# Performance work log

Measured on AMD Instinct MI355X. Metric: run time of the kernel, lower is better.

The kernel has to match this reference:

```python
import jax, jax.numpy as jnp
import numpy as np

H, DD, NCLS, NELEM, NPROP = 256, 32, 8, 11, 14
B, N = 4, 4096
ENC = NELEM + NPROP  # 25

_DIMS = [("dc1", ENC, H), ("dc21", H, DD), ("dc22", H, DD),
         ("in1", ENC, H), ("in2", H, H), ("in3", H, H),
         ("conv", H, H),
         ("id1", H, H), ("id2", H, H), ("id3", H, H),
         ("oid", H, NCLS), ("och", H, 2),
         ("m1", H + NCLS, H + NCLS), ("m2", H + NCLS, H), ("m3", H, H), ("om", H, 3)]


def setup_inputs() -> dict:
    key = jax.random.key(0)
    ks = jax.random.split(key, 2 + len(_DIMS))
    X = jax.random.normal(ks[0], (B, N, 15), jnp.float32)
    ids = jax.random.randint(ks[1], (B, N), 0, NELEM).astype(jnp.float32)
    X = X.at[:, :, 0].set(ids)
    d = {"X": X}
    for i, (name, di, do) in enumerate(_DIMS):
        W = jax.random.normal(ks[2 + i], (di, do), jnp.float32) / np.sqrt(di)
        d["W_" + name] = W
        d["b_" + name] = jnp.zeros((do,), jnp.float32)
    return d


def reference(X, W_dc1, b_dc1, W_dc21, b_dc21, W_dc22, b_dc22,
              W_in1, b_in1, W_in2, b_in2, W_in3, b_in3,
              W_conv, b_conv,
              W_id1, b_id1, W_id2, b_id2, W_id3, b_id3,
              W_oid, b_oid, W_och, b_och,
              W_m1, b_m1, W_m2, b_m2, W_m3, b_m3, W_om, b_om):
    act = jax.nn.selu
    # input encoding: one-hot element id (stop-grad via int cast) + properties, then selu
    onehot = jax.nn.one_hot(X[:, :, 0].astype(jnp.int32), NELEM, dtype=X.dtype)
    enc = act(jnp.concatenate([onehot, X[:, :, 1:]], axis=-1))  # [B,N,25]
    # distance coordinates
    h = act(enc @ W_dc1 + b_dc1)
    c1 = h @ W_dc21 + b_dc21  # [B,N,DD]
    c2 = h @ W_dc22 + b_dc22
    # pairwise distance -> exp adjacency
    na = jnp.sum(c1 * c1, -1)[:, :, None]
    nb = jnp.sum(c2 * c2, -1)[:, None, :]
    Dsq = jnp.clip(na - 2.0 * jnp.einsum('bnd,bmd->bnm', c1, c2) + nb, 1e-12, 1e12)
    adj = jnp.exp(-jnp.sqrt(Dsq))  # [B,N,N]
    # node MLP
    x = act(enc @ W_in1 + b_in1)
    x = act(x @ W_in2 + b_in2)
    x = act(x @ W_in3 + b_in3)
    # GraphConv: adj^k @ (x W) + b, k=4 (in-degree norm computed but unused upstream)
    x = act(jnp.einsum('bnm,bmh->bnh', adj ** 4, x @ W_conv) + b_conv)
    # id head
    a = act(x @ W_id1 + b_id1)
    a = act(a @ W_id2 + b_id2)
    a = act(a @ W_id3 + b_id3)
    out_id_logits = a @ W_oid + b_oid  # [B,N,8]
    out_charge = a @ W_och + b_och     # [B,N,2]
    # momentum head
    xb = jnp.concatenate([x, act(out_id_logits)], axis=-1)
    bb = act(xb @ W_m1 + b_m1)
    bb = act(bb @ W_m2 + b_m2)
    bb = act(bb @ W_m3 + b_m3)
    corr = bb @ W_om + b_om  # [B,N,3]
    mom = jnp.stack([X[:, :, 2] + corr[:, :, 0],
                     X[:, :, 3] + corr[:, :, 1],
                     X[:, :, 4] + corr[:, :, 2]], axis=-1)
    return jnp.concatenate([out_id_logits, mom, out_charge], axis=-1)  # [B,N,13]
```

## Files before the change

### kernel.cpp

```cpp
#include <hip/hip_runtime.h>
#include <cstddef>
#include <cstdint>

#define MROWS 16384
#define NSEQ  4096
#define ASTR  296
#define SELU_SCALE  1.0507009873554805f
#define SELU_ASCALE 1.7580993408473766f

typedef short bf16x8 __attribute__((ext_vector_type(8)));
typedef float f32x4  __attribute__((ext_vector_type(4)));

__device__ __forceinline__ float selu_f(float x) {
    return x > 0.f ? SELU_SCALE * x : SELU_ASCALE * (__expf(x) - 1.f);
}
__device__ __forceinline__ unsigned short f2bf(float x) {
    union { float f; unsigned int u; } v; v.f = x;
    unsigned int r = v.u + 0x7fffu + ((v.u >> 16) & 1u);
    return (unsigned short)(r >> 16);
}
__device__ __forceinline__ unsigned short t2bf(float x) {
    union { float f; unsigned int u; } v; v.f = x;
    return (unsigned short)(v.u >> 16);
}

struct PrepEnt { const float* W; unsigned short* WTf; int N, K, ntiles, KS, tileOff, tilesN; };
struct PrepArgs {
    PrepEnt e[16];
    const float *b21, *b22, *boid, *boch, *bdc1, *bin1;
    float *bc12, *boo, *bcat;
};
__global__ __launch_bounds__(256) void prep_kernel(PrepArgs pa) {
    if (blockIdx.y == 1) {
        if (blockIdx.x == 0) {
            int t = threadIdx.x;
            if (t < 32) pa.bc12[t] = pa.b21[t];
            else if (t < 64) pa.bc12[t] = pa.b22[t - 32];
            else if (t < 96) {
                int j = t - 64;
                pa.boo[j] = j < 8 ? pa.boid[j] : ((j >= 16 && j < 18) ? pa.boch[j - 16] : 0.f);
            }
        } else if (blockIdx.x == 1) {
            pa.bcat[threadIdx.x] = pa.bdc1[threadIdx.x];
        } else if (blockIdx.x == 2) {
            pa.bcat[256 + threadIdx.x] = pa.bin1[threadIdx.x];
        }
        return;
    }
    int bx = blockIdx.x;
    int ei = 0;
#pragma unroll
    for (int e = 1; e < 16; ++e)
        if (bx >= pa.e[e].tileOff) ei = e;
    PrepEnt E = pa.e[ei];
    int local = bx - E.tileOff;
    int tn = local / E.KS, tk = local - tn * E.KS;
    int k0 = tk * 32, n0 = tn * 32;

    __shared__ float ts[32][33];
    int t = threadIdx.x;
    {
        int kl = t >> 3, nl4 = (t & 7) * 4;
        int gk = k0 + kl;
#pragma unroll
        for (int j = 0; j < 4; ++j) {
            int gn = n0 + nl4 + j;
            float v = (gk < E.K && gn < E.N) ? E.W[(size_t)gk * E.N + gn] : 0.f;
            ts[nl4 + j][kl] = v;
        }
    }
    __syncthreads();
    int nl = t >> 3, kl4 = (t & 7) * 4;
    int n = n0 + nl;
    if (n < E.ntiles * 16) {
        ushort4 o;
        o.x = f2bf(ts[nl][kl4 + 0]);
        o.y = f2bf(ts[nl][kl4 + 1]);
        o.z = f2bf(ts[nl][kl4 + 2]);
        o.w = f2bf(ts[nl][kl4 + 3]);
        size_t dst = ((size_t)(n >> 4) * E.KS + tk) * 512 +
                     (size_t)((kl4 >> 3) * 16 + (n & 15)) * 8 + (kl4 & 7);
        *(ushort4*)(E.WTf + dst) = o;
    }
}

template <int MT, int NT>
__device__ __forceinline__ void zero_acc(f32x4 (&acc)[MT][NT]) {
#pragma unroll
    for (int i = 0; i < MT; ++i)
#pragma unroll
        for (int nt = 0; nt < NT; ++nt) acc[i][nt] = (f32x4){0.f, 0.f, 0.f, 0.f};
}

template <int MT, int NT, int K>
__device__ __forceinline__ void compute_tiles(
    f32x4 (&acc)[MT][NT],
    const unsigned short* __restrict__ src, int sstr,
    const unsigned short* __restrict__ WTf,
    int col0, int ln)
{
    constexpr int KS = (K + 31) / 32;
    int quad = ln >> 4, l15 = ln & 15;
    const unsigned short* wp = WTf + (size_t)(col0 >> 4) * (KS * 512) + ln * 8;
    bf16x8 st[3][NT];
#pragma unroll
    for (int s = 0; s < 3; ++s) {
        if (s < KS) {
#pragma unroll
            for (int nt = 0; nt < NT; ++nt)
                st[s][nt] = *(const bf16x8*)(wp + nt * (KS * 512) + s * 512);
        }
    }
#pragma unroll
    for (int ks = 0; ks < KS; ++ks) {
        bf16x8 bnew[NT];
        if (ks + 3 < KS) {
#pragma unroll
            for (int nt = 0; nt < NT; ++nt)
                bnew[nt] = *(const bf16x8*)(wp + nt * (KS * 512) + (ks + 3) * 512);
        }
#pragma unroll
        for (int i = 0; i < MT; ++i) {
            bf16x8 af = *(const bf16x8*)(src + (i * 16 + l15) * sstr + ks * 32 + quad * 8);
#pragma unroll
            for (int nt = 0; nt < NT; ++nt)
                acc[i][nt] = __builtin_amdgcn_mfma_f32_16x16x32_bf16(af, st[ks % 3][nt], acc[i][nt], 0, 0, 0);
        }
        if (ks + 3 < KS) {
#pragma unroll
            for (int nt = 0; nt < NT; ++nt) st[ks % 3][nt] = bnew[nt];
        }
    }
}

template <int MT, int NT>
__device__ __forceinline__ void store_tiles(
    f32x4 (&acc)[MT][NT], unsigned short* __restrict__ dst,
    int col0, const float* __restrict__ bias, int Nreal, int act, int ln)
{
    int quad = ln >> 4, l15 = ln & 15;
#pragma unroll
    for (int nt = 0; nt < NT; ++nt) {
        int col = col0 + nt * 16 + l15;
        float bv = (bias && col < Nreal) ? bias[col] : 0.f;
#pragma unroll
        for (int i = 0; i < MT; ++i) {
#pragma unroll
            for (int r = 0; r < 4; ++r) {
                int row = i * 16 + quad * 4 + r;
                float v = acc[i][nt][r] + bv;
                if (act) v = selu_f(v);
                if (col >= Nreal) v = 0.f;
                dst[row * ASTR + col] = f2bf(v);
            }
        }
    }
}

__global__ __launch_bounds__(512, 6) void pre_mega(
    const float* __restrict__ X,
    const unsigned short* __restrict__ WTdF, const float* __restrict__ bcat,
    const unsigned short* __restrict__ WTc12F, const float* __restrict__ bc12,
    const unsigned short* __restrict__ WTin2F, const float* __restrict__ b_in2,
    const unsigned short* __restrict__ WTin3F, const float* __restrict__ b_in3,
    const unsigned short* __restrict__ WTconvF,
    unsigned short* __restrict__ c1b, unsigned short* __restrict__ c2b,
    float* __restrict__ n1, float* __restrict__ n2,
    unsigned short* __restrict__ xwTb)
{
    __shared__ unsigned short encs[32 * 32];
    __shared__ unsigned short bufA[32 * ASTR];
    __shared__ unsigned short bufB[32 * ASTR];
    __shared__ float c12s[32 * 68];

    int tid = threadIdx.x, wv = tid >> 6, ln = tid & 63;
    int quad = ln >> 4, l15 = ln & 15;
    int row0 = blockIdx.x * 32;

#pragma unroll
    for (int p = 0; p < 2; ++p) {
        int idx = p * 512 + tid;
        int row = idx >> 5, col = idx & 31;
        float v = 0.f;
        if (col < 11) {
            int id = (int)X[(size_t)(row0 + row) * 15];
            v = (id == col) ? SELU_SCALE : 0.f;
        } else if (col < 25) {
            v = selu_f(X[(size_t)(row0 + row) * 15 + 1 + (col - 11)]);
        }
        encs[row * 32 + col] = f2bf(v);
    }
    __syncthreads();

#pragma unroll
    for (int ph = 0; ph < 2; ++ph) {
        f32x4 acc[2][2]; zero_acc<2, 2>(acc);
        compute_tiles<2, 2, 32>(acc, encs, 32, WTdF + (size_t)ph * 16 * 512, wv * 32, ln);
        store_tiles<2, 2>(acc, ph ? bufB : bufA, wv * 32, bcat + ph * 256, 256, 1, ln);
    }
    __syncthreads();

    f32x4 ax2[2][2]; zero_acc<2, 2>(ax2);
    compute_tiles<2, 2, 256>(ax2, bufB, ASTR, WTin2F, wv * 32, ln);
    f32x4 ac12[2][1];
    if (wv < 4) {
        zero_acc<2, 1>(ac12);
        compute_tiles<2, 1, 256>(ac12, bufA, ASTR, WTc12F, wv * 16, ln);
    }
    __syncthreads();
    store_tiles<2, 2>(ax2, bufA, wv * 32, b_in2, 256, 1, ln);
    if (wv < 4) {
        int col = wv * 16 + l15;
        float bv = bc12[col];
#pragma unroll
        for (int i = 0; i < 2; ++i)
#pragma unroll
            for (int r = 0; r < 4; ++r)
                c12s[(i * 16 + quad * 4 + r) * 68 + col] = ac12[i][0][r] + bv;
    }
    __syncthreads();

    if (tid < 32) {
        int grow = row0 + tid;
        const float* p = &c12s[tid * 68];
        float s1 = 0.f, s2 = 0.f;
        unsigned int o1[16], o2[16];
#pragma unroll
        for (int k = 0; k < 32; k += 2) {
            float a0 = p[k], a1 = p[k + 1];
            s1 += a0 * a0 + a1 * a1;
            o1[k >> 1] = (unsigned)f2bf(a0) | ((unsigned)f2bf(a1) << 16);
            float b0 = p[32 + k], b1 = p[33 + k];
            s2 += b0 * b0 + b1 * b1;
            o2[k >> 1] = (unsigned)f2bf(b0) | ((unsigned)f2bf(b1) << 16);
        }
        uint4* d1 = (uint4*)(c1b + (size_t)grow * 32);
        uint4* d2 = (uint4*)(c2b + (size_t)grow * 32);
#pragma unroll
        for (int j = 0; j < 4; ++j) {
            d1[j] = make_uint4(o1[4 * j], o1[4 * j + 1], o1[4 * j + 2], o1[4 * j + 3]);
            d2[j] = make_uint4(o2[4 * j], o2[4 * j + 1], o2[4 * j + 2], o2[4 * j + 3]);
        }
        n1[grow] = s1;
        n2[grow] = s2;
    }

    {
        f32x4 acc[2][2]; zero_acc<2, 2>(acc);
        compute_tiles<2, 2, 256>(acc, bufA, ASTR, WTin3F, wv * 32, ln);
        store_tiles<2, 2>(acc, bufB, wv * 32, b_in3, 256, 1, ln);
    }
    __syncthreads();
    {
        f32x4 acc[2][2]; zero_acc<2, 2>(acc);
        compute_tiles<2, 2, 256>(acc, bufB, ASTR, WTconvF, wv * 32, ln);
        store_tiles<2, 2>(acc, bufA, wv * 32, nullptr, 256, 0, ln);
    }
    __syncthreads();

    int b = row0 >> 12;
    int c0 = (row0 & 4095) >> 5;
    unsigned short* dst = xwTb + (size_t)(b * 128 + c0) * (256 * 32);
#pragma unroll
    for (int p = 0; p < 2; ++p) {
        int idx = p * 512 + tid;
        int h = idx >> 2, g = idx & 3;
        unsigned int w[4];
#pragma unroll
        for (int j = 0; j < 4; ++j) {
            unsigned int lo = bufA[(g * 8 + 2 * j) * ASTR + h];
            unsigned int hi = bufA[(g * 8 + 2 * j + 1) * ASTR + h];
            w[j] = lo | (hi << 16);
        }
        *(uint4*)(dst + (size_t)h * 32 + g * 8) = make_uint4(w[0], w[1], w[2], w[3]);
    }
}

__global__ __launch_bounds__(512, 4) void adj_conv_mfma(
    const unsigned short* __restrict__ c1b, const unsigned short* __restrict__ c2b,
    const float* __restrict__ n1, const float* __restrict__ n2,
    const unsigned short* __restrict__ xwTb, const float* __restrict__ bconv,
    unsigned short* __restrict__ xc)
{
    __shared__ unsigned short wls[2][32][136];

    int tid = threadIdx.x, wv = tid >> 6, ln = tid & 63, quad = ln >> 4, l15 = ln & 15;
    int blk = blockIdx.x;
    int b = (blk >> 1) & 3;
    int iidx = ((blk >> 3) << 1) | (blk & 1);
    int i0 = iidx * 32;
    size_t base = (size_t)b * NSEQ;

    bf16x8 c1f0 = *(const bf16x8*)(c1b + (base + i0 + l15) * 32 + quad * 8);
    bf16x8 c1f1 = *(const bf16x8*)(c1b + (base + i0 + 16 + l15) * 32 + quad * 8);
    float4 n1v0 = *(const float4*)(n1 + base + i0 + quad * 4);
    float4 n1v1 = *(const float4*)(n1 + base + i0 + 16 + quad * 4);

    const unsigned short* xwp0 = xwTb + (size_t)b * (128 * 256 * 32)
                               + ((size_t)(wv * 32 + l15) * 32 + quad * 8);
    const unsigned short* xwp1 = xwp0 + 8192;
    const unsigned short* xwp2 = xwp0 + 16384;
    const unsigned short* xwp3 = xwp0 + 24576;
    const unsigned short* c2p  = c2b + (base + wv * 16 + l15) * 32 + quad * 8;
    const float* n2p = n2 + base + wv * 16 + l15;

    f32x4 acc[2][2];
#pragma unroll
    for (int i = 0; i < 2; ++i)
#pragma unroll
        for (int j = 0; j < 2; ++j) acc[i][j] = (f32x4){0.f, 0.f, 0.f, 0.f};

    bf16x8 c2f = *(const bf16x8*)c2p;
    float nn2 = *n2p;
    c2p += 4096; n2p += 128;
    {
        f32x4 d0 = (f32x4){0.f, 0.f, 0.f, 0.f};
        f32x4 d1 = (f32x4){0.f, 0.f, 0.f, 0.f};
        d0 = __builtin_amdgcn_mfma_f32_16x16x32_bf16(c1f0, c2f, d0, 0, 0, 0);
        d1 = __builtin_amdgcn_mfma_f32_16x16x32_bf16(c1f1, c2f, d1, 0, 0, 0);
#pragma unroll
        for (int r = 0; r < 4; ++r) {
            float D0 = fmaf(-2.f, d0[r], n1v0[r] + nn2);
            float D1 = fmaf(-2.f, d1[r], n1v1[r] + nn2);
            float t0 = __builtin_amdgcn_sqrtf(fmaxf(D0, 1e-12f));
            float t1 = __builtin_amdgcn_sqrtf(fmaxf(D1, 1e-12f));
            wls[0][quad * 4 + r][wv * 16 + l15]      = t2bf(__expf(t0 * -4.f));
            wls[0][16 + quad * 4 + r][wv * 16 + l15] = t2bf(__expf(t1 * -4.f));
        }
    }
    c2f = *(const bf16x8*)c2p;
    nn2 = *n2p;
    c2p += 4096; n2p += 128;
    __syncthreads();

    for (int itr = 0; itr < 32; ++itr) {
        int p = itr & 1;
        bf16x8 bfc[4][2];
#pragma unroll
        for (int ht = 0; ht < 2; ++ht) {
            bfc[0][ht] = *(const bf16x8*)(xwp0 + ht * 512);
            bfc[1][ht] = *(const bf16x8*)(xwp1 + ht * 512);
            bfc[2][ht] = *(const bf16x8*)(xwp2 + ht * 512);
            bfc[3][ht] = *(const bf16x8*)(xwp3 + ht * 512);
        }
        xwp0 += 32768; xwp1 += 32768; xwp2 += 32768; xwp3 += 32768;

        if (itr < 31) {
            f32x4 d0 = (f32x4){0.f, 0.f, 0.f, 0.f};
            f32x4 d1 = (f32x4){0.f, 0.f, 0.f, 0.f};
            d0 = __builtin_amdgcn_mfma_f32_16x16x32_bf16(c1f0, c2f, d0, 0, 0, 0);
            d1 = __builtin_amdgcn_mfma_f32_16x16x32_bf16(c1f1, c2f, d1, 0, 0, 0);
            bf16x8 c2n; float nnn;
            if (itr < 30) {
                c2n = *(const bf16x8*)c2p;
                nnn = *n2p;
                c2p += 4096; n2p += 128;
            }
#pragma unroll
            for (int r = 0; r < 4; ++r) {
                float D0 = fmaf(-2.f, d0[r], n1v0[r] + nn2);
                float D1 = fmaf(-2.f, d1[r], n1v1[r] + nn2);
                float t0 = __builtin_amdgcn_sqrtf(fmaxf(D0, 1e-12f));
                float t1 = __builtin_amdgcn_sqrtf(fmaxf(D1, 1e-12f));
                wls[p ^ 1][quad * 4 + r][wv * 16 + l15]      = t2bf(__expf(t0 * -4.f));
                wls[p ^ 1][16 + quad * 4 + r][wv * 16 + l15] = t2bf(__expf(t1 * -4.f));
            }
            if (itr < 30) { c2f = c2n; nn2 = nnn; }
        }

#pragma unroll
        for (int ks = 0; ks < 4; ++ks) {
            bf16x8 af0 = *(const bf16x8*)&wls[p][l15][ks * 32 + quad * 8];
            bf16x8 af1 = *(const bf16x8*)&wls[p][16 + l15][ks * 32 + quad * 8];
            acc[0][0] = __builtin_amdgcn_mfma_f32_16x16x32_bf16(af0, bfc[ks][0], acc[0][0], 0, 0, 0);
            acc[0][1] = __builtin_amdgcn_mfma_f32_16x16x32_bf16(af0, bfc[ks][1], acc[0][1], 0, 0, 0);
            acc[1][0] = __builtin_amdgcn_mfma_f32_16x16x32_bf16(af1, bfc[ks][0], acc[1][0], 0, 0, 0);
            acc[1][1] = __builtin_amdgcn_mfma_f32_16x16x32_bf16(af1, bfc[ks][1], acc[1][1], 0, 0, 0);
        }
        __syncthreads();
    }

#pragma unroll
    for (int mi = 0; mi < 2; ++mi) {
#pragma unroll
        for (int ht = 0; ht < 2; ++ht) {
            int h = wv * 32 + ht * 16 + l15;
            float bv = bconv[h];
#pragma unroll
            for (int r = 0; r < 4; ++r) {
                int irow = i0 + mi * 16 + quad * 4 + r;
                xc[(base + irow) * 256 + h] = f2bf(selu_f(acc[mi][ht][r] + bv));
            }
        }
    }
}

__global__ __launch_bounds__(512, 4) void post_mega(
    const float* __restrict__ X, const unsigned short* __restrict__ xc,
    const unsigned short* __restrict__ WTid1F, const float* __restrict__ b_id1,
    const unsigned short* __restrict__ WTid2F, const float* __restrict__ b_id2,
    const unsigned short* __restrict__ WTid3F, const float* __restrict__ b_id3,
    const unsigned short* __restrict__ WTooF, const float* __restrict__ boo,
    const unsigned short* __restrict__ WTm1F, const float* __restrict__ b_m1,
    const unsigned short* __restrict__ WTm2F, const float* __restrict__ b_m2,
    const unsigned short* __restrict__ WTm3F, const float* __restrict__ b_m3,
    const unsigned short* __restrict__ WTomF, const float* __restrict__ b_om,
    float* __restrict__ out)
{
    __shared__ unsigned short xcs[32 * ASTR];
    __shared__ unsigned short bufA[32 * ASTR];
    __shared__ unsigned short bufB[32 * ASTR];
    __shared__ float lgs[32 * 32];

    int tid = threadIdx.x, wv = tid >> 6, ln = tid & 63;
    int quad = ln >> 4, l15 = ln & 15;
    int row0 = blockIdx.x * 32;

#pragma unroll
    for (int p = 0; p < 2; ++p) {
        int idx = p * 512 + tid;
        int row = idx >> 5, c8 = (idx & 31) * 8;
        *(uint4*)&xcs[row * ASTR + c8] = *(const uint4*)(xc + (size_t)(row0 + row) * 256 + c8);
    }
#pragma unroll
    for (int p = 0; p < 3; ++p) {
        int idx = p * 512 + tid;
        if (idx < 1280) {
            int row = idx / 40, c = 256 + idx - row * 40;
            xcs[row * ASTR + c] = 0;
            bufB[row * ASTR + c] = 0;
        }
    }
    __syncthreads();

    {
        f32x4 acc[2][2]; zero_acc<2, 2>(acc);
        compute_tiles<2, 2, 256>(acc, xcs, ASTR, WTid1F, wv * 32, ln);
        store_tiles<2, 2>(acc, bufA, wv * 32, b_id1, 256, 1, ln);
    }
    __syncthreads();
    {
        f32x4 acc[2][2]; zero_acc<2, 2>(acc);
        compute_tiles<2, 2, 256>(acc, bufA, ASTR, WTid2F, wv * 32, ln);
        store_tiles<2, 2>(acc, bufB, wv * 32, b_id2, 256, 1, ln);
    }
    __syncthreads();
    {
        f32x4 acc[2][2]; zero_acc<2, 2>(acc);
        compute_tiles<2, 2, 256>(acc, bufB, ASTR, WTid3F, wv * 32, ln);
        store_tiles<2, 2>(acc, bufA, wv * 32, b_id3, 256, 1, ln);
    }
    __syncthreads();
    if (wv == 0) {
        f32x4 acc[2][2]; zero_acc<2, 2>(acc);
        compute_tiles<2, 2, 256>(acc, bufA, ASTR, WTooF, 0, ln);
#pragma unroll
        for (int nt = 0; nt < 2; ++nt) {
            int col = nt * 16 + l15;
            float bv = boo[col];
#pragma unroll
            for (int i = 0; i < 2; ++i)
#pragma unroll
                for (int r = 0; r < 4; ++r)
                    lgs[(i * 16 + quad * 4 + r) * 32 + col] = acc[i][nt][r] + bv;
        }
    }
    __syncthreads();
    if (tid < 32) {
        float* op = out + (size_t)(row0 + tid) * 13;
#pragma unroll
        for (int c = 0; c < 8; ++c) {
            float lg = lgs[tid * 32 + c];
            op[c] = lg;
            xcs[tid * ASTR + 256 + c] = f2bf(selu_f(lg));
        }
        op[11] = lgs[tid * 32 + 16];
        op[12] = lgs[tid * 32 + 17];
    }
    __syncthreads();
    {
        f32x4 acc[2][2]; zero_acc<2, 2>(acc);
        compute_tiles<2, 2, 288>(acc, xcs, ASTR, WTm1F, wv * 32, ln);
        store_tiles<2, 2>(acc, bufB, wv * 32, b_m1, 264, 1, ln);
        if (wv == 1) {
            f32x4 acx[2][1]; zero_acc<2, 1>(acx);
            compute_tiles<2, 1, 288>(acx, xcs, ASTR, WTm1F, 256, ln);
            store_tiles<2, 1>(acx, bufB, 256, b_m1, 264, 1, ln);
        }
    }
    __syncthreads();
    {
        f32x4 acc[2][2]; zero_acc<2, 2>(acc);
        compute_tiles<2, 2, 288>(acc, bufB, ASTR, WTm2F, wv * 32, ln);
        store_tiles<2, 2>(acc, bufA, wv * 32, b_m2, 256, 1, ln);
    }
    __syncthreads();
    {
        f32x4 acc[2][2]; zero_acc<2, 2>(acc);
        compute_tiles<2, 2, 256>(acc, bufA, ASTR, WTm3F, wv * 32, ln);
        store_tiles<2, 2>(acc, bufB, wv * 32, b_m3, 256, 1, ln);
    }
    __syncthreads();
    if (wv == 0) {
        f32x4 acc[2][1]; zero_acc<2, 1>(acc);
        compute_tiles<2, 1, 256>(acc, bufB, ASTR, WTomF, 0, ln);
        if (l15 < 3) {
            float bv = b_om[l15];
#pragma unroll
            for (int i = 0; i < 2; ++i)
#pragma unroll
                for (int r = 0; r < 4; ++r) {
                    int grow = row0 + i * 16 + quad * 4 + r;
                    out[(size_t)grow * 13 + 8 + l15] =
                        X[(size_t)grow * 15 + 2 + l15] + acc[i][0][r] + bv;
                }
        }
    }
}

extern "C" void kernel_launch(void* const* d_in, const int* in_sizes, int n_in,
                              void* d_out, int out_size, void* d_ws, size_t ws_size,
                              hipStream_t stream) {
    (void)in_sizes; (void)n_in; (void)out_size; (void)ws_size;

    const float* X = (const float*)d_in[0];
    const float* W_dc1 = (const float*)d_in[1];  const float* b_dc1 = (const float*)d_in[2];
    const float* W_dc21 = (const float*)d_in[3]; const float* b_dc21 = (const float*)d_in[4];
    const float* W_dc22 = (const float*)d_in[5]; const float* b_dc22 = (const float*)d_in[6];
    const float* W_in1 = (const float*)d_in[7];  const float* b_in1 = (const float*)d_in[8];
    const float* W_in2 = (const float*)d_in[9];  const float* b_in2 = (const float*)d_in[10];
    const float* W_in3 = (const float*)d_in[11]; const float* b_in3 = (const float*)d_in[12];
    const float* W_conv = (const float*)d_in[13]; const float* b_conv = (const float*)d_in[14];
    const float* W_id1 = (const float*)d_in[15]; const float* b_id1 = (const float*)d_in[16];
    const float* W_id2 = (const float*)d_in[17]; const float* b_id2 = (const float*)d_in[18];
    const float* W_id3 = (const float*)d_in[19]; const float* b_id3 = (const float*)d_in[20];
    const float* W_oid = (const float*)d_in[21]; const float* b_oid = (const float*)d_in[22];
    const float* W_och = (const float*)d_in[23]; const float* b_och = (const float*)d_in[24];
    const float* W_m1 = (const float*)d_in[25];  const float* b_m1 = (const float*)d_in[26];
    const float* W_m2 = (const float*)d_in[27];  const float* b_m2 = (const float*)d_in[28];
    const float* W_m3 = (const float*)d_in[29];  const float* b_m3 = (const float*)d_in[30];
    const float* W_om = (const float*)d_in[31];  const float* b_om = (const float*)d_in[32];

    const size_t M = MROWS;
    char* pw = (char*)d_ws;
    auto alloc = [&](size_t bytes) -> void* {
        void* r = (void*)pw;
        pw += (bytes + 255) & ~(size_t)255;
        return r;
    };
    unsigned short* c1b = (unsigned short*)alloc(M * 32 * 2);
    unsigned short* c2b = (unsigned short*)alloc(M * 32 * 2);
    float* n1 = (float*)alloc(M * 4);
    float* n2 = (float*)alloc(M * 4);
    unsigned short* xwTb = (unsigned short*)alloc((size_t)4 * 128 * 256 * 32 * 2);
    unsigned short* xcb = (unsigned short*)alloc(M * 256 * 2);
    unsigned short* WTdF   = (unsigned short*)alloc((size_t)2 * 16 * 1 * 512 * 2);
    unsigned short* WTc12F = (unsigned short*)alloc((size_t)4 * 8 * 512 * 2);
    unsigned short* WTin2F = (unsigned short*)alloc((size_t)16 * 8 * 512 * 2);
    unsigned short* WTin3F = (unsigned short*)alloc((size_t)16 * 8 * 512 * 2);
    unsigned short* WTconvF = (unsigned short*)alloc((size_t)16 * 8 * 512 * 2);
    unsigned short* WTid1F = (unsigned short*)alloc((size_t)16 * 8 * 512 * 2);
    unsigned short* WTid2F = (unsigned short*)alloc((size_t)16 * 8 * 512 * 2);
    unsigned short* WTid3F = (unsigned short*)alloc((size_t)16 * 8 * 512 * 2);
    unsigned short* WTm3F  = (unsigned short*)alloc((size_t)16 * 8 * 512 * 2);
    unsigned short* WTooF  = (unsigned short*)alloc((size_t)2 * 8 * 512 * 2);
    unsigned short* WTm1F  = (unsigned short*)alloc((size_t)17 * 9 * 512 * 2);
    unsigned short* WTm2F  = (unsigned short*)alloc((size_t)16 * 9 * 512 * 2);
    unsigned short* WTomF  = (unsigned short*)alloc((size_t)1 * 8 * 512 * 2);
    float* bc12 = (float*)alloc(64 * 4);
    float* boo = (float*)alloc(32 * 4);
    float* bcat = (float*)alloc(512 * 4);

    PrepArgs pa;
    int off = 0;
    auto ent = [&](const float* W, unsigned short* WTf, int N, int K, int ntiles) {
        PrepEnt e; e.W = W; e.WTf = WTf; e.N = N; e.K = K; e.ntiles = ntiles;
        e.KS = (K + 31) / 32;
        e.tilesN = (ntiles * 16 + 31) / 32;
        e.tileOff = off;
        off += e.tilesN * e.KS;
        return e;
    };
    pa.e[0]  = ent(W_dc1,  WTdF,                256, 25,  16);
    pa.e[1]  = ent(W_in1,  WTdF + 16 * 512,     256, 25,  16);
    pa.e[2]  = ent(W_dc21, WTc12F,              32,  256, 2);
    pa.e[3]  = ent(W_dc22, WTc12F + 2 * 8 * 512, 32, 256, 2);
    pa.e[4]  = ent(W_in2,  WTin2F,              256, 256, 16);
    pa.e[5]  = ent(W_in3,  WTin3F,              256, 256, 16);
    pa.e[6]  = ent(W_conv, WTconvF,             256, 256, 16);
    pa.e[7]  = ent(W_id1,  WTid1F,              256, 256, 16);
    pa.e[8]  = ent(W_id2,  WTid2F,              256, 256, 16);
    pa.e[9]  = ent(W_id3,  WTid3F,              256, 256, 16);
    pa.e[10] = ent(W_m3,   WTm3F,               256, 256, 16);
    pa.e[11] = ent(W_oid,  WTooF,               8,   256, 1);
    pa.e[12] = ent(W_och,  WTooF + 8 * 512,     2,   256, 1);
    pa.e[13] = ent(W_m1,   WTm1F,               264, 264, 17);
    pa.e[14] = ent(W_m2,   WTm2F,               256, 264, 16);
    pa.e[15] = ent(W_om,   WTomF,               3,   256, 1);
    pa.b21 = b_dc21; pa.b22 = b_dc22; pa.boid = b_oid; pa.boch = b_och;
    pa.bdc1 = b_dc1; pa.bin1 = b_in1;
    pa.bc12 = bc12; pa.boo = boo; pa.bcat = bcat;
    prep_kernel<<<dim3(off, 2), 256, 0, stream>>>(pa);

    pre_mega<<<dim3(512), 512, 0, stream>>>(X, WTdF, bcat, WTc12F, bc12,
                                            WTin2F, b_in2, WTin3F, b_in3, WTconvF,
                                            c1b, c2b, n1, n2, xwTb);

    adj_conv_mfma<<<dim3(512), 512, 0, stream>>>(c1b, c2b, n1, n2, xwTb, b_conv, xcb);

    post_mega<<<dim3(512), 512, 0, stream>>>(X, xcb,
                                             WTid1F, b_id1, WTid2F, b_id2, WTid3F, b_id3,
                                             WTooF, boo, WTm1F, b_m1, WTm2F, b_m2,
                                             WTm3F, b_m3, WTomF, b_om, (float*)d_out);
}
```

Baseline: 241.5 us.

## Fuse adjacency-conv kernel with post-MLP heads into one kernel

Merges the adjacency/graph-conv kernel and the post MLP kernel so each block keeps its 32 conv output rows in shared memory and runs the id and momentum heads directly. This removes the global write and read of the 16384x256 bf16 intermediate and one kernel launch. In exchange, shared memory per block grows a lot (conv staging buffers plus three activation buffers), which can lower occupancy during the dominant N^2 adjacency phase.

```diff
diff --git a/kernel.cpp b/kernel.cpp
--- a/kernel.cpp
+++ b/kernel.cpp
@@ -276,13 +276,26 @@
     }
 }
 
-__global__ __launch_bounds__(512, 4) void adj_conv_mfma(
+__global__ __launch_bounds__(512, 4) void adj_post(
     const unsigned short* __restrict__ c1b, const unsigned short* __restrict__ c2b,
     const float* __restrict__ n1, const float* __restrict__ n2,
     const unsigned short* __restrict__ xwTb, const float* __restrict__ bconv,
-    unsigned short* __restrict__ xc)
+    const float* __restrict__ X,
+    const unsigned short* __restrict__ WTid1F, const float* __restrict__ b_id1,
+    const unsigned short* __restrict__ WTid2F, const float* __restrict__ b_id2,
+    const unsigned short* __restrict__ WTid3F, const float* __restrict__ b_id3,
+    const unsigned short* __restrict__ WTooF, const float* __restrict__ boo,
+    const unsigned short* __restrict__ WTm1F, const float* __restrict__ b_m1,
+    const unsigned short* __restrict__ WTm2F, const float* __restrict__ b_m2,
+    const unsigned short* __restrict__ WTm3F, const float* __restrict__ b_m3,
+    const unsigned short* __restrict__ WTomF, const float* __restrict__ b_om,
+    float* __restrict__ out)
 {
     __shared__ unsigned short wls[2][32][136];
+    __shared__ unsigned short xcs[32 * ASTR];
+    __shared__ unsigned short bufA[32 * ASTR];
+    __shared__ unsigned short bufB[32 * ASTR];
+    __shared__ float lgs[32 * 32];
 
     int tid = threadIdx.x, wv = tid >> 6, ln = tid & 63, quad = ln >> 4, l15 = ln & 15;
     int blk = blockIdx.x;
@@ -290,6 +303,17 @@
     int iidx = ((blk >> 3) << 1) | (blk & 1);
     int i0 = iidx * 32;
     size_t base = (size_t)b * NSEQ;
+    size_t grow0 = base + i0;
+
+#pragma unroll
+    for (int p = 0; p < 3; ++p) {
+        int idx = p * 512 + tid;
+        if (idx < 1280) {
+            int row = idx / 40, c = 256 + idx - row * 40;
+            xcs[row * ASTR + c] = 0;
+            bufB[row * ASTR + c] = 0;
+        }
+    }
 
     bf16x8 c1f0 = *(const bf16x8*)(c1b + (base + i0 + l15) * 32 + quad * 8);
     bf16x8 c1f1 = *(const bf16x8*)(c1b + (base + i0 + 16 + l15) * 32 + quad * 8);
@@ -388,72 +412,34 @@
             float bv = bconv[h];
 #pragma unroll
             for (int r = 0; r < 4; ++r) {
-                int irow = i0 + mi * 16 + quad * 4 + r;
-                xc[(base + irow) * 256 + h] = f2bf(selu_f(acc[mi][ht][r] + bv));
+                int lrow = mi * 16 + quad * 4 + r;
+                xcs[lrow * ASTR + h] = f2bf(selu_f(acc[mi][ht][r] + bv));
             }
         }
     }
-}
-
-__global__ __launch_bounds__(512, 4) void post_mega(
-    const float* __restrict__ X, const unsigned short* __restrict__ xc,
-    const unsigned short* __restrict__ WTid1F, const float* __restrict__ b_id1,
-    const unsigned short* __restrict__ WTid2F, const float* __restrict__ b_id2,
-    const unsigned short* __restrict__ WTid3F, const float* __restrict__ b_id3,
-    const unsigned short* __restrict__ WTooF, const float* __restrict__ boo,
-    const unsigned short* __restrict__ WTm1F, const float* __restrict__ b_m1,
-    const unsigned short* __restrict__ WTm2F, const float* __restrict__ b_m2,
-    const unsigned short* __restrict__ WTm3F, const float* __restrict__ b_m3,
-    const unsigned short* __restrict__ WTomF, const float* __restrict__ b_om,
-    float* __restrict__ out)
-{
-    __shared__ unsigned short xcs[32 * ASTR];
-    __shared__ unsigned short bufA[32 * ASTR];
-    __shared__ unsigned short bufB[32 * ASTR];
-    __shared__ float lgs[32 * 32];
-
-    int tid = threadIdx.x, wv = tid >> 6, ln = tid & 63;
-    int quad = ln >> 4, l15 = ln & 15;
-    int row0 = blockIdx.x * 32;
-
-#pragma unroll
-    for (int p = 0; p < 2; ++p) {
-        int idx = p * 512 + tid;
-        int row = idx >> 5, c8 = (idx & 31) * 8;
-        *(uint4*)&xcs[row * ASTR + c8] = *(const uint4*)(xc + (size_t)(row0 + row) * 256 + c8);
-    }
-#pragma unroll
-    for (int p = 0; p < 3; ++p) {
-        int idx = p * 512 + tid;
-        if (idx < 1280) {
-            int row = idx / 40, c = 256 + idx - row * 40;
-            xcs[row * ASTR + c] = 0;
-            bufB[row * ASTR + c] = 0;
-        }
-    }
-    __syncthreads();
-
-    {
-        f32x4 acc[2][2]; zero_acc<2, 2>(acc);
-        compute_tiles<2, 2, 256>(acc, xcs, ASTR, WTid1F, wv * 32, ln);
-        store_tiles<2, 2>(acc, bufA, wv * 32, b_id1, 256, 1, ln);
-    }
-    __syncthreads();
-    {
-        f32x4 acc[2][2]; zero_acc<2, 2>(acc);
-        compute_tiles<2, 2, 256>(acc, bufA, ASTR, WTid2F, wv * 32, ln);
-        store_tiles<2, 2>(acc, bufB, wv * 32, b_id2, 256, 1, ln);
-    }
-    __syncthreads();
-    {
-        f32x4 acc[2][2]; zero_acc<2, 2>(acc);
-        compute_tiles<2, 2, 256>(acc, bufB, ASTR, WTid3F, wv * 32, ln);
-        store_tiles<2, 2>(acc, bufA, wv * 32, b_id3, 256, 1, ln);
+    __syncthreads();
+
+    {
+        f32x4 a2[2][2]; zero_acc<2, 2>(a2);
+        compute_tiles<2, 2, 256>(a2, xcs, ASTR, WTid1F, wv * 32, ln);
+        store_tiles<2, 2>(a2, bufA, wv * 32, b_id1, 256, 1, ln);
+    }
+    __syncthreads();
+    {
+        f32x4 a2[2][2]; zero_acc<2, 2>(a2);
+        compute_tiles<2, 2, 256>(a2, bufA, ASTR, WTid2F, wv * 32, ln);
+        store_tiles<2, 2>(a2, bufB, wv * 32, b_id2, 256, 1, ln);
+    }
+    __syncthreads();
+    {
+        f32x4 a2[2][2]; zero_acc<2, 2>(a2);
+        compute_tiles<2, 2, 256>(a2, bufB, ASTR, WTid3F, wv * 32, ln);
+        store_tiles<2, 2>(a2, bufA, wv * 32, b_id3, 256, 1, ln);
     }
     __syncthreads();
     if (wv == 0) {
-        f32x4 acc[2][2]; zero_acc<2, 2>(acc);
-        compute_tiles<2, 2, 256>(acc, bufA, ASTR, WTooF, 0, ln);
+        f32x4 a2[2][2]; zero_acc<2, 2>(a2);
+        compute_tiles<2, 2, 256>(a2, bufA, ASTR, WTooF, 0, ln);
 #pragma unroll
         for (int nt = 0; nt < 2; ++nt) {
             int col = nt * 16 + l15;
@@ -462,12 +448,12 @@
             for (int i = 0; i < 2; ++i)
 #pragma unroll
                 for (int r = 0; r < 4; ++r)
-                    lgs[(i * 16 + quad * 4 + r) * 32 + col] = acc[i][nt][r] + bv;
+                    lgs[(i * 16 + quad * 4 + r) * 32 + col] = a2[i][nt][r] + bv;
         }
     }
     __syncthreads();
     if (tid < 32) {
-        float* op = out + (size_t)(row0 + tid) * 13;
+        float* op = out + (grow0 + tid) * 13;
 #pragma unroll
         for (int c = 0; c < 8; ++c) {
             float lg = lgs[tid * 32 + c];
@@ -479,9 +465,9 @@
     }
     __syncthreads();
     {
-        f32x4 acc[2][2]; zero_acc<2, 2>(acc);
-        compute_tiles<2, 2, 288>(acc, xcs, ASTR, WTm1F, wv * 32, ln);
-        store_tiles<2, 2>(acc, bufB, wv * 32, b_m1, 264, 1, ln);
+        f32x4 a2[2][2]; zero_acc<2, 2>(a2);
+        compute_tiles<2, 2, 288>(a2, xcs, ASTR, WTm1F, wv * 32, ln);
+        store_tiles<2, 2>(a2, bufB, wv * 32, b_m1, 264, 1, ln);
         if (wv == 1) {
             f32x4 acx[2][1]; zero_acc<2, 1>(acx);
             compute_tiles<2, 1, 288>(acx, xcs, ASTR, WTm1F, 256, ln);
@@ -490,29 +476,29 @@
     }
     __syncthreads();
     {
-        f32x4 acc[2][2]; zero_acc<2, 2>(acc);
-        compute_tiles<2, 2, 288>(acc, bufB, ASTR, WTm2F, wv * 32, ln);
-        store_tiles<2, 2>(acc, bufA, wv * 32, b_m2, 256, 1, ln);
-    }
-    __syncthreads();
-    {
-        f32x4 acc[2][2]; zero_acc<2, 2>(acc);
-        compute_tiles<2, 2, 256>(acc, bufA, ASTR, WTm3F, wv * 32, ln);
-        store_tiles<2, 2>(acc, bufB, wv * 32, b_m3, 256, 1, ln);
+        f32x4 a2[2][2]; zero_acc<2, 2>(a2);
+        compute_tiles<2, 2, 288>(a2, bufB, ASTR, WTm2F, wv * 32, ln);
+        store_tiles<2, 2>(a2, bufA, wv * 32, b_m2, 256, 1, ln);
+    }
+    __syncthreads();
+    {
+        f32x4 a2[2][2]; zero_acc<2, 2>(a2);
+        compute_tiles<2, 2, 256>(a2, bufA, ASTR, WTm3F, wv * 32, ln);
+        store_tiles<2, 2>(a2, bufB, wv * 32, b_m3, 256, 1, ln);
     }
     __syncthreads();
     if (wv == 0) {
-        f32x4 acc[2][1]; zero_acc<2, 1>(acc);
-        compute_tiles<2, 1, 256>(acc, bufB, ASTR, WTomF, 0, ln);
+        f32x4 a2[2][1]; zero_acc<2, 1>(a2);
+        compute_tiles<2, 1, 256>(a2, bufB, ASTR, WTomF, 0, ln);
         if (l15 < 3) {
             float bv = b_om[l15];
 #pragma unroll
             for (int i = 0; i < 2; ++i)
 #pragma unroll
                 for (int r = 0; r < 4; ++r) {
-                    int grow = row0 + i * 16 + quad * 4 + r;
-                    out[(size_t)grow * 13 + 8 + l15] =
-                        X[(size_t)grow * 15 + 2 + l15] + acc[i][0][r] + bv;
+                    size_t grow = grow0 + i * 16 + quad * 4 + r;
+                    out[grow * 13 + 8 + l15] =
+                        X[grow * 15 + 2 + l15] + a2[i][0][r] + bv;
                 }
         }
     }
@@ -553,7 +539,6 @@
     float* n1 = (float*)alloc(M * 4);
     float* n2 = (float*)alloc(M * 4);
     unsigned short* xwTb = (unsigned short*)alloc((size_t)4 * 128 * 256 * 32 * 2);
-    unsigned short* xcb = (unsigned short*)alloc(M * 256 * 2);
     unsigned short* WTdF   = (unsigned short*)alloc((size_t)2 * 16 * 1 * 512 * 2);
     unsigned short* WTc12F = (unsigned short*)alloc((size_t)4 * 8 * 512 * 2);
     unsigned short* WTin2F = (unsigned short*)alloc((size_t)16 * 8 * 512 * 2);
@@ -606,10 +591,8 @@
                                             WTin2F, b_in2, WTin3F, b_in3, WTconvF,
                                             c1b, c2b, n1, n2, xwTb);
 
-    adj_conv_mfma<<<dim3(512), 512, 0, stream>>>(c1b, c2b, n1, n2, xwTb, b_conv, xcb);
-
-    post_mega<<<dim3(512), 512, 0, stream>>>(X, xcb,
-                                             WTid1F, b_id1, WTid2F, b_id2, WTid3F, b_id3,
-                                             WTooF, boo, WTm1F, b_m1, WTm2F, b_m2,
-                                             WTm3F, b_m3, WTomF, b_om, (float*)d_out);
-}
+    adj_post<<<dim3(512), 512, 0, stream>>>(c1b, c2b, n1, n2, xwTb, b_conv, X,
+                                            WTid1F, b_id1, WTid2F, b_id2, WTid3F, b_id3,
+                                            WTooF, boo, WTm1F, b_m1, WTm2F, b_m2,
+                                            WTm3F, b_m3, WTomF, b_om, (float*)d_out);
+}
```

New measurement: 234.4 us. 2.9% less time.
